# Optimization experiments

Hardware: AMD Instinct MI355X
Metric: run time of the kernel (lower is better)

Reference implementation:

```python
import jax, jax.numpy as jnp
import numpy as np

BH, S, D = 16, 2048, 128  # batch*heads, seq_len, head_dim


def setup_inputs() -> dict:
    key = jax.random.key(0)
    kq, kk, kv = jax.random.split(key, 3)
    q = jax.random.normal(kq, (BH, S, D), dtype=jnp.float32)
    k = jax.random.normal(kk, (BH, S, D), dtype=jnp.float32)
    v = jax.random.normal(kv, (BH, S, D), dtype=jnp.float32)
    # causal mask, True = masked (matches torch masked_fill_ semantics);
    # broadcast to the required [BH, S, S] shape per the module's assert.
    causal = jnp.triu(jnp.ones((S, S), dtype=jnp.bool_), k=1)
    attn_mask = jnp.broadcast_to(causal, (BH, S, S))
    return {"q": q, "k": k, "v": v, "attn_mask": attn_mask}


def reference(q, k, v, attn_mask):
    # NOTE: original module applies NO 1/sqrt(d) scaling despite its name.
    attn = jnp.einsum("bqd,bkd->bqk", q, k)              # [BH, S, S]
    attn = jnp.where(attn_mask, -jnp.inf, attn)
    attn = jax.nn.softmax(attn, axis=-1)
    # dropout is identity in eval mode
    out = jnp.einsum("bqk,bkd->bqd", attn, v)            # [BH, S, D]
    return out * q, attn                                  # faithful quirk: output * q
```

## Files before the change

### kernel.cpp

```cpp
#include <hip/hip_runtime.h>

#define BH_ 16
#define S_ 2048
#define D_ 128
#define KB_ 64
#define QB_ 64

typedef __attribute__((ext_vector_type(4))) float f32x4;
typedef __attribute__((ext_vector_type(8))) short bf16x8;
typedef unsigned short ushort_t;

__device__ __forceinline__ unsigned short f2bf(float x) {
  union { float f; unsigned int u; } v; v.f = x;
  unsigned int r = v.u + 0x7fffu + ((v.u >> 16) & 1u);
  return (unsigned short)(r >> 16);
}
__device__ __forceinline__ float bf2f(unsigned short b) {
  union { float f; unsigned int u; } v; v.u = ((unsigned int)b) << 16;
  return v.f;
}

__global__ __launch_bounds__(256) void convKfrag(const float* __restrict__ K,
                                                 ushort_t* __restrict__ KH,
                                                 ushort_t* __restrict__ KL) {
  const int tid = threadIdx.x;
  const int seg = tid >> 6;
  const int tl  = tid & 63;
  const int kt = blockIdx.x, bh = blockIdx.y;
  const float* src0 = K + ((size_t)bh * S_ + kt * 64 + (tl & 15)) * D_ +
                      seg * 32 + (tl >> 4) * 8;
  char* dh = (char*)KH + ((size_t)(bh * 32 + kt) * 16 + seg * 4) * 1024 + tl * 16;
  char* dl = (char*)KL + ((size_t)(bh * 32 + kt) * 16 + seg * 4) * 1024 + tl * 16;
#pragma unroll
  for (int t = 0; t < 4; ++t) {
    const float* src = src0 + (size_t)t * 16 * D_;
    float4 a = *(const float4*)src;
    float4 b = *(const float4*)(src + 4);
    float xs[8] = {a.x, a.y, a.z, a.w, b.x, b.y, b.z, b.w};
    union { ushort_t u[8]; uint4 v; } H, L;
#pragma unroll
    for (int j = 0; j < 8; ++j) {
      unsigned short h = f2bf(xs[j]);
      H.u[j] = h;
      L.u[j] = f2bf(xs[j] - bf2f(h));
    }
    *(uint4*)(dh + t * 1024) = H.v;
    *(uint4*)(dl + t * 1024) = L.v;
  }
}

__global__ __launch_bounds__(256) void convVfrag(const float* __restrict__ V,
                                                 ushort_t* __restrict__ VF) {
  __shared__ ushort_t tile[64][136];
  const int tid = threadIdx.x;
  const int kt = blockIdx.x, bh = blockIdx.y;
  const float* Vb = V + ((size_t)bh * S_ + kt * 64) * D_;
#pragma unroll
  for (int it = 0; it < 8; ++it) {
    int idx = it * 256 + tid;
    int fl = idx * 4;
    int s = fl >> 7, d = fl & 127;
    float4 f = *(const float4*)(Vb + (size_t)s * D_ + d);
    tile[s][d + 0] = f2bf(f.x);
    tile[s][d + 1] = f2bf(f.y);
    tile[s][d + 2] = f2bf(f.z);
    tile[s][d + 3] = f2bf(f.w);
  }
  __syncthreads();
  char* dst0 = (char*)VF + (size_t)(bh * 32 + kt) * 16384;
#pragma unroll
  for (int j = 0; j < 4; ++j) {
    int ci = j * 256 + tid;
    int l = ci & 63, fid = ci >> 6;
    int ks = fid >> 3, dt = fid & 7;
    int s0 = ks * 32 + (l >> 4) * 8;
    int d = dt * 16 + (l & 15);
    union { ushort_t u[8]; uint4 v; } T;
#pragma unroll
    for (int i = 0; i < 8; ++i) T.u[i] = tile[s0 + i][d];
    *(uint4*)(dst0 + (size_t)fid * 1024 + l * 16) = T.v;
  }
}

__global__ __launch_bounds__(256) void sdpa_fused(
    const float* __restrict__ Q, const ushort_t* __restrict__ KH,
    const ushort_t* __restrict__ KL, const ushort_t* __restrict__ VF,
    float* __restrict__ out, float* __restrict__ attn) {
  __shared__ ushort_t els[32 * 1024];
  __shared__ float rsLDS[4][16];

  const int tid = threadIdx.x, w = tid >> 6, lane = tid & 63;
  const int g = lane >> 4, c = lane & 15;

  const int bid = blockIdx.x;
  const int xcd = bid & 7, slot = bid >> 3;
  const int bh = xcd + 8 * (slot >> 7);
  const int rt = 127 - (slot & 127);
  const int q0 = rt * 16;
  const int nk = (rt >> 2) + 1;

  const float* Qb = Q + (size_t)bh * S_ * D_;
  const char* KHb = (const char*)KH + (size_t)bh * 32 * 16384;
  const char* KLb = (const char*)KL + (size_t)bh * 32 * 16384;
  const char* VFb = (const char*)VF + (size_t)bh * 32 * 16384;
  float* outb  = out  + (size_t)bh * S_ * D_;
  float* attnb = attn + (size_t)bh * S_ * S_;

  bf16x8 qhi[4], qlo[4];
  {
    const float* qrow = Qb + (size_t)(q0 + c) * D_;
#pragma unroll
    for (int ch = 0; ch < 4; ++ch) {
      const float* src = qrow + ch * 32 + g * 8;
      float4 a = *(const float4*)src;
      float4 b = *(const float4*)(src + 4);
      float xs[8] = {a.x, a.y, a.z, a.w, b.x, b.y, b.z, b.w};
#pragma unroll
      for (int i = 0; i < 8; ++i) {
        unsigned short h = f2bf(xs[i]);
        qhi[ch][i] = (short)h;
        qlo[ch][i] = (short)f2bf(xs[i] - bf2f(h));
      }
    }
  }

  const f32x4 zero4 = {0.f, 0.f, 0.f, 0.f};
  f32x4 oacc[8];
  float rs[4] = {0.f, 0.f, 0.f, 0.f};
#pragma unroll
  for (int dt = 0; dt < 8; ++dt) oacc[dt] = zero4;

  for (int kt = w; kt < nk; kt += 4) {
    const char* kth = KHb + (size_t)kt * 16384 + lane * 16;
    const char* ktl = KLb + (size_t)kt * 16384 + lane * 16;
    const char* ktv = VFb + (size_t)kt * 16384 + lane * 16;

    f32x4 acc[4];
#pragma unroll
    for (int t = 0; t < 4; ++t) acc[t] = zero4;
#pragma unroll
    for (int c2 = 0; c2 < 4; ++c2) {
      bf16x8 kh[4], kl[4];
#pragma unroll
      for (int t = 0; t < 4; ++t) {
        kh[t] = *(const bf16x8*)(kth + (c2 * 4 + t) * 1024);
        kl[t] = *(const bf16x8*)(ktl + (c2 * 4 + t) * 1024);
      }
#pragma unroll
      for (int t = 0; t < 4; ++t)
        acc[t] = __builtin_amdgcn_mfma_f32_16x16x32_bf16(qhi[c2], kh[t], acc[t], 0, 0, 0);
#pragma unroll
      for (int t = 0; t < 4; ++t)
        acc[t] = __builtin_amdgcn_mfma_f32_16x16x32_bf16(qlo[c2], kh[t], acc[t], 0, 0, 0);
#pragma unroll
      for (int t = 0; t < 4; ++t)
        acc[t] = __builtin_amdgcn_mfma_f32_16x16x32_bf16(qhi[c2], kl[t], acc[t], 0, 0, 0);
    }

#pragma unroll
    for (int r2 = 0; r2 < 4; ++r2) {
      int qrow = g * 4 + r2;
      int qg = q0 + qrow;
#pragma unroll
      for (int t = 0; t < 4; ++t) {
        int kc = t * 16 + c;
        int kg = kt * 64 + kc;
        float e = (kg <= qg) ? __expf(acc[t][r2]) : 0.f;
        rs[r2] += e;
        int off = kt * 2048 + qrow * 128 + ((kc * 2) ^ ((qrow & 7) << 4));
        *(ushort_t*)((char*)els + off) = f2bf(e);
      }
    }

    bf16x8 pa[2];
#pragma unroll
    for (int ks = 0; ks < 2; ++ks) {
      int off = kt * 2048 + c * 128 + ((ks * 64 + g * 16) ^ ((c & 7) << 4));
      pa[ks] = *(const bf16x8*)((const char*)els + off);
    }
#pragma unroll
    for (int ks = 0; ks < 2; ++ks) {
#pragma unroll
      for (int dt = 0; dt < 8; ++dt) {
        bf16x8 vf = *(const bf16x8*)(ktv + (ks * 8 + dt) * 1024);
        oacc[dt] = __builtin_amdgcn_mfma_f32_16x16x32_bf16(pa[ks], vf, oacc[dt], 0, 0, 0);
      }
    }
  }

#pragma unroll
  for (int r2 = 0; r2 < 4; ++r2) {
    float s0 = rs[r2];
#pragma unroll
    for (int m = 1; m <= 8; m <<= 1) s0 += __shfl_xor(s0, m, 64);
    if (c == 0) rsLDS[w][g * 4 + r2] = s0;
  }
  __syncthreads();

  {
    float ivr[4];
#pragma unroll
    for (int rr = 0; rr < 4; ++rr) {
      int r = w * 4 + rr;
      ivr[rr] = 1.0f / (rsLDS[0][r] + rsLDS[1][r] + rsLDS[2][r] + rsLDS[3][r]);
    }
#pragma unroll
    for (int rr = 0; rr < 4; ++rr) {
      const int r = w * 4 + rr;
      const float iv = ivr[rr];
      float* arow = attnb + (size_t)(q0 + r) * S_;
#pragma unroll
      for (int it = 0; it < 4; ++it) {
        int kb8 = it * 512 + lane * 8;
        float4 o0, o1;
        if ((kb8 >> 6) < nk) {
          const char* src = (const char*)els + (kb8 >> 6) * 2048 + r * 128 +
                            (((kb8 & 63) * 2) ^ ((r & 7) << 4));
          bf16x8 ev = *(const bf16x8*)src;
          o0.x = bf2f((ushort_t)ev[0]) * iv; o0.y = bf2f((ushort_t)ev[1]) * iv;
          o0.z = bf2f((ushort_t)ev[2]) * iv; o0.w = bf2f((ushort_t)ev[3]) * iv;
          o1.x = bf2f((ushort_t)ev[4]) * iv; o1.y = bf2f((ushort_t)ev[5]) * iv;
          o1.z = bf2f((ushort_t)ev[6]) * iv; o1.w = bf2f((ushort_t)ev[7]) * iv;
        } else {
          o0 = make_float4(0.f, 0.f, 0.f, 0.f);
          o1 = o0;
        }
        *(float4*)(arow + kb8) = o0;
        *(float4*)(arow + kb8 + 4) = o1;
      }
    }
  }
  __syncthreads();

  if (w > 0) {
    char* base = (char*)els + (size_t)(w - 1) * 8192 + lane * 128;
#pragma unroll
    for (int dt = 0; dt < 8; ++dt)
      *(f32x4*)(base + ((dt * 16) ^ ((lane & 7) << 4))) = oacc[dt];
  }
  __syncthreads();
  if (w == 0) {
    float ivr2[4];
#pragma unroll
    for (int r2 = 0; r2 < 4; ++r2) {
      int r = g * 4 + r2;
      ivr2[r2] = 1.0f / (rsLDS[0][r] + rsLDS[1][r] + rsLDS[2][r] + rsLDS[3][r]);
    }
#pragma unroll
    for (int dt = 0; dt < 8; ++dt) {
      f32x4 o = oacc[dt];
#pragma unroll
      for (int j = 0; j < 3; ++j)
        o += *(const f32x4*)((const char*)els + (size_t)j * 8192 + lane * 128 +
                             ((dt * 16) ^ ((lane & 7) << 4)));
      int d = dt * 16 + c;
#pragma unroll
      for (int r2 = 0; r2 < 4; ++r2) {
        int qg = q0 + g * 4 + r2;
        outb[(size_t)qg * D_ + d] = o[r2] * ivr2[r2] * Qb[(size_t)qg * D_ + d];
      }
    }
  }
}

__global__ __launch_bounds__(256, 2)
void sdpa_fallback(const float* __restrict__ Q, const float* __restrict__ K,
                   const float* __restrict__ V, float* __restrict__ out,
                   float* __restrict__ attn)
{
  __shared__ unsigned short khi[KB_ * D_];
  __shared__ unsigned short klo[KB_ * D_];
  __shared__ unsigned short vts[D_ * KB_];
  __shared__ unsigned short pls[4][16 * KB_];

  const int tid  = threadIdx.x;
  const int w    = tid >> 6;
  const int lane = tid & 63;
  const int g    = lane >> 4;
  const int c    = lane & 15;

  const int bh = blockIdx.y;
  const int qb = (int)gridDim.x - 1 - (int)blockIdx.x;
  const int q0 = qb * QB_;

  const float* Qb = Q + (size_t)bh * S_ * D_;
  const float* Kb = K + (size_t)bh * S_ * D_;
  const float* Vb = V + (size_t)bh * S_ * D_;
  float* outb  = out  + (size_t)bh * S_ * D_;
  float* attnb = attn + (size_t)bh * S_ * S_;

  {
    const int colstart = q0 + QB_;
    for (int r = 0; r < QB_; ++r) {
      float* rowp = attnb + (size_t)(q0 + r) * S_;
      for (int col = colstart + tid * 4; col < S_; col += 1024)
        *(float4*)(rowp + col) = make_float4(0.f, 0.f, 0.f, 0.f);
    }
  }

  bf16x8 qhi[4], qlo[4];
  {
    const float* qrow = Qb + (size_t)(q0 + w * 16 + c) * D_;
#pragma unroll
    for (int ch = 0; ch < 4; ++ch) {
      const float* src = qrow + ch * 32 + g * 8;
      float4 a = *(const float4*)src;
      float4 b = *(const float4*)(src + 4);
      float xs[8] = {a.x, a.y, a.z, a.w, b.x, b.y, b.z, b.w};
#pragma unroll
      for (int i = 0; i < 8; ++i) {
        unsigned short h = f2bf(xs[i]);
        unsigned short l = f2bf(xs[i] - bf2f(h));
        qhi[ch][i] = (short)h;
        qlo[ch][i] = (short)l;
      }
    }
  }

  auto stageK = [&](int kb) {
#pragma unroll
    for (int rr = 0; rr < 8; ++rr) {
      int flat = tid * 4 + rr * 1024;
      int kj = flat >> 7, d0 = flat & 127;
      const float* src = Kb + (size_t)(kb * KB_ + kj) * D_ + d0;
      float4 f = *(const float4*)src;
      unsigned short h0 = f2bf(f.x), h1 = f2bf(f.y), h2 = f2bf(f.z), h3 = f2bf(f.w);
      unsigned short l0 = f2bf(f.x - bf2f(h0)), l1 = f2bf(f.y - bf2f(h1));
      unsigned short l2 = f2bf(f.z - bf2f(h2)), l3 = f2bf(f.w - bf2f(h3));
      int off = kj * 256 + ((d0 * 2) ^ ((kj & 7) << 4));
      *(uint2*)((char*)khi + off) =
          make_uint2((unsigned)h0 | ((unsigned)h1 << 16), (unsigned)h2 | ((unsigned)h3 << 16));
      *(uint2*)((char*)klo + off) =
          make_uint2((unsigned)l0 | ((unsigned)l1 << 16), (unsigned)l2 | ((unsigned)l3 << 16));
    }
  };

  const f32x4 zero4 = {0.f, 0.f, 0.f, 0.f};
  auto computeS = [&](f32x4* acc) {
#pragma unroll
    for (int t = 0; t < 4; ++t) {
      acc[t] = zero4;
      int row = t * 16 + c;
      int rbase = row * 256;
      int sw = (row & 7) << 4;
#pragma unroll
      for (int c2 = 0; c2 < 4; ++c2) {
        int off = rbase + ((c2 * 64 + g * 16) ^ sw);
        bf16x8 kh_ = *(const bf16x8*)((const char*)khi + off);
        bf16x8 kl_ = *(const bf16x8*)((const char*)klo + off);
        acc[t] = __builtin_amdgcn_mfma_f32_16x16x32_bf16(qhi[c2], kh_, acc[t], 0, 0, 0);
        acc[t] = __builtin_amdgcn_mfma_f32_16x16x32_bf16(qhi[c2], kl_, acc[t], 0, 0, 0);
        acc[t] = __builtin_amdgcn_mfma_f32_16x16x32_bf16(qlo[c2], kh_, acc[t], 0, 0, 0);
      }
    }
  };

  float rsum[4] = {0.f, 0.f, 0.f, 0.f};
  for (int kb = 0; kb <= qb; ++kb) {
    __syncthreads();
    stageK(kb);
    __syncthreads();
    f32x4 acc[4];
    computeS(acc);
#pragma unroll
    for (int r2 = 0; r2 < 4; ++r2) {
      int qg = q0 + w * 16 + g * 4 + r2;
      float s0 = 0.f;
#pragma unroll
      for (int t = 0; t < 4; ++t) {
        int kg = kb * KB_ + t * 16 + c;
        float e = (kg <= qg) ? __expf(acc[t][r2]) : 0.f;
        s0 += e;
      }
#pragma unroll
      for (int m = 1; m <= 8; m <<= 1) s0 += __shfl_xor(s0, m, 64);
      rsum[r2] += s0;
    }
  }
  float invl[4];
#pragma unroll
  for (int r2 = 0; r2 < 4; ++r2) invl[r2] = 1.0f / rsum[r2];

  f32x4 oacc[8];
#pragma unroll
  for (int dt = 0; dt < 8; ++dt) oacc[dt] = zero4;

  for (int kb = 0; kb <= qb; ++kb) {
    __syncthreads();
    stageK(kb);
#pragma unroll
    for (int rr = 0; rr < 8; ++rr) {
      int d0 = 4 * (w + 4 * rr);
      const float* src = Vb + (size_t)(kb * KB_ + lane) * D_ + d0;
      float4 f = *(const float4*)src;
      float xs[4] = {f.x, f.y, f.z, f.w};
#pragma unroll
      for (int i = 0; i < 4; ++i) {
        int d = d0 + i;
        int off = d * 128 + ((lane * 2) ^ ((d & 7) << 4));
        *(unsigned short*)((char*)vts + off) = f2bf(xs[i]);
      }
    }
    __syncthreads();

    f32x4 acc[4];
    computeS(acc);

#pragma unroll
    for (int r2 = 0; r2 < 4; ++r2) {
      int qrow = g * 4 + r2;
      int qg = q0 + w * 16 + qrow;
#pragma unroll
      for (int t = 0; t < 4; ++t) {
        int kc = t * 16 + c;
        int kg = kb * KB_ + kc;
        float p = (kg <= qg) ? __expf(acc[t][r2]) * invl[r2] : 0.f;
        attnb[(size_t)qg * S_ + kg] = p;
        int off = qrow * 128 + ((kc * 2) ^ ((qrow & 7) << 4));
        *(unsigned short*)((char*)pls[w] + off) = f2bf(p);
      }
    }
    __syncthreads();

    bf16x8 pa[2];
#pragma unroll
    for (int ks = 0; ks < 2; ++ks) {
      int off = c * 128 + ((ks * 64 + g * 16) ^ ((c & 7) << 4));
      pa[ks] = *(const bf16x8*)((const char*)pls[w] + off);
    }
#pragma unroll
    for (int dt = 0; dt < 8; ++dt) {
      int d = dt * 16 + c;
      int rbase = d * 128;
      int sw = (d & 7) << 4;
#pragma unroll
      for (int ks = 0; ks < 2; ++ks) {
        int off = rbase + ((ks * 64 + g * 16) ^ sw);
        bf16x8 vf = *(const bf16x8*)((const char*)vts + off);
        oacc[dt] = __builtin_amdgcn_mfma_f32_16x16x32_bf16(pa[ks], vf, oacc[dt], 0, 0, 0);
      }
    }
  }

#pragma unroll
  for (int dt = 0; dt < 8; ++dt) {
#pragma unroll
    for (int r2 = 0; r2 < 4; ++r2) {
      int qg = q0 + w * 16 + g * 4 + r2;
      int d = dt * 16 + c;
      float qv = Qb[(size_t)qg * D_ + d];
      outb[(size_t)qg * D_ + d] = oacc[dt][r2] * qv;
    }
  }
}

extern "C" void kernel_launch(void* const* d_in, const int* in_sizes, int n_in,
                              void* d_out, int out_size, void* d_ws, size_t ws_size,
                              hipStream_t stream) {
  const float* q = (const float*)d_in[0];
  const float* k = (const float*)d_in[1];
  const float* v = (const float*)d_in[2];
  float* out  = (float*)d_out;
  float* attn = out + (size_t)BH_ * S_ * D_;

  const size_t nKV = (size_t)BH_ * S_ * D_;
  const size_t need = nKV * 2 * 3;

  if (ws_size >= need) {
    ushort_t* KH = (ushort_t*)d_ws;
    ushort_t* KL = KH + nKV;
    ushort_t* VF = KL + nKV;

    convKfrag<<<dim3(S_ / 64, BH_), dim3(256), 0, stream>>>(k, KH, KL);
    convVfrag<<<dim3(S_ / 64, BH_), dim3(256), 0, stream>>>(v, VF);
    sdpa_fused<<<dim3(BH_ * 128), dim3(256), 0, stream>>>(q, KH, KL, VF, out, attn);
  } else {
    sdpa_fallback<<<dim3(S_ / QB_, BH_), dim3(256), 0, stream>>>(q, k, v, out, attn);
  }
}
```

Before: 133.4 us.

## Use 32-row query tiles with paired causal rows in 512-thread blocks

Replaces the 16-row, 4-wave fused attention kernel with a 32-row, 8-wave kernel. Each block processes two query tiles, p and 63-p, so causal work is balanced across a fixed grid of 512 blocks. Each K fragment loaded from global memory now feeds two 16-row MFMA groups, which halves K traffic per query row. The output reduction across waves is moved to an LDS park-and-sum with vectorised float4 stores. In exchange, the kernel uses 128KB of LDS, which probably limits it to one block per CU despite the launch bound, and it adds extra barriers per tile.

```diff
diff --git a/kernel.cpp b/kernel.cpp
--- a/kernel.cpp
+++ b/kernel.cpp
@@ -82,22 +82,19 @@
   }
 }
 
-__global__ __launch_bounds__(256) void sdpa_fused(
+__global__ __launch_bounds__(512, 2) void sdpa_fused32(
     const float* __restrict__ Q, const ushort_t* __restrict__ KH,
     const ushort_t* __restrict__ KL, const ushort_t* __restrict__ VF,
     float* __restrict__ out, float* __restrict__ attn) {
-  __shared__ ushort_t els[32 * 1024];
-  __shared__ float rsLDS[4][16];
+  __shared__ ushort_t els[65536];
+  __shared__ float rsLDS[8][32];
 
   const int tid = threadIdx.x, w = tid >> 6, lane = tid & 63;
   const int g = lane >> 4, c = lane & 15;
 
   const int bid = blockIdx.x;
-  const int xcd = bid & 7, slot = bid >> 3;
-  const int bh = xcd + 8 * (slot >> 7);
-  const int rt = 127 - (slot & 127);
-  const int q0 = rt * 16;
-  const int nk = (rt >> 2) + 1;
+  const int bh = (bid & 7) + 8 * ((bid >> 3) & 1);
+  const int p = bid >> 4;
 
   const float* Qb = Q + (size_t)bh * S_ * D_;
   const char* KHb = (const char*)KH + (size_t)bh * 32 * 16384;
@@ -106,115 +103,140 @@
   float* outb  = out  + (size_t)bh * S_ * D_;
   float* attnb = attn + (size_t)bh * S_ * S_;
 
-  bf16x8 qhi[4], qlo[4];
-  {
-    const float* qrow = Qb + (size_t)(q0 + c) * D_;
-#pragma unroll
-    for (int ch = 0; ch < 4; ++ch) {
-      const float* src = qrow + ch * 32 + g * 8;
-      float4 a = *(const float4*)src;
-      float4 b = *(const float4*)(src + 4);
-      float xs[8] = {a.x, a.y, a.z, a.w, b.x, b.y, b.z, b.w};
-#pragma unroll
-      for (int i = 0; i < 8; ++i) {
-        unsigned short h = f2bf(xs[i]);
-        qhi[ch][i] = (short)h;
-        qlo[ch][i] = (short)f2bf(xs[i] - bf2f(h));
-      }
-    }
-  }
-
   const f32x4 zero4 = {0.f, 0.f, 0.f, 0.f};
-  f32x4 oacc[8];
-  float rs[4] = {0.f, 0.f, 0.f, 0.f};
-#pragma unroll
-  for (int dt = 0; dt < 8; ++dt) oacc[dt] = zero4;
-
-  for (int kt = w; kt < nk; kt += 4) {
-    const char* kth = KHb + (size_t)kt * 16384 + lane * 16;
-    const char* ktl = KLb + (size_t)kt * 16384 + lane * 16;
-    const char* ktv = VFb + (size_t)kt * 16384 + lane * 16;
-
-    f32x4 acc[4];
-#pragma unroll
-    for (int t = 0; t < 4; ++t) acc[t] = zero4;
-#pragma unroll
-    for (int c2 = 0; c2 < 4; ++c2) {
-      bf16x8 kh[4], kl[4];
-#pragma unroll
-      for (int t = 0; t < 4; ++t) {
-        kh[t] = *(const bf16x8*)(kth + (c2 * 4 + t) * 1024);
-        kl[t] = *(const bf16x8*)(ktl + (c2 * 4 + t) * 1024);
-      }
-#pragma unroll
-      for (int t = 0; t < 4; ++t)
-        acc[t] = __builtin_amdgcn_mfma_f32_16x16x32_bf16(qhi[c2], kh[t], acc[t], 0, 0, 0);
-#pragma unroll
-      for (int t = 0; t < 4; ++t)
-        acc[t] = __builtin_amdgcn_mfma_f32_16x16x32_bf16(qlo[c2], kh[t], acc[t], 0, 0, 0);
-#pragma unroll
-      for (int t = 0; t < 4; ++t)
-        acc[t] = __builtin_amdgcn_mfma_f32_16x16x32_bf16(qhi[c2], kl[t], acc[t], 0, 0, 0);
-    }
-
-#pragma unroll
-    for (int r2 = 0; r2 < 4; ++r2) {
-      int qrow = g * 4 + r2;
-      int qg = q0 + qrow;
-#pragma unroll
-      for (int t = 0; t < 4; ++t) {
-        int kc = t * 16 + c;
-        int kg = kt * 64 + kc;
-        float e = (kg <= qg) ? __expf(acc[t][r2]) : 0.f;
-        rs[r2] += e;
-        int off = kt * 2048 + qrow * 128 + ((kc * 2) ^ ((qrow & 7) << 4));
-        *(ushort_t*)((char*)els + off) = f2bf(e);
-      }
-    }
-
-    bf16x8 pa[2];
-#pragma unroll
-    for (int ks = 0; ks < 2; ++ks) {
-      int off = kt * 2048 + c * 128 + ((ks * 64 + g * 16) ^ ((c & 7) << 4));
-      pa[ks] = *(const bf16x8*)((const char*)els + off);
-    }
-#pragma unroll
-    for (int ks = 0; ks < 2; ++ks) {
-#pragma unroll
-      for (int dt = 0; dt < 8; ++dt) {
-        bf16x8 vf = *(const bf16x8*)(ktv + (ks * 8 + dt) * 1024);
-        oacc[dt] = __builtin_amdgcn_mfma_f32_16x16x32_bf16(pa[ks], vf, oacc[dt], 0, 0, 0);
-      }
-    }
-  }
-
-#pragma unroll
-  for (int r2 = 0; r2 < 4; ++r2) {
-    float s0 = rs[r2];
-#pragma unroll
-    for (int m = 1; m <= 8; m <<= 1) s0 += __shfl_xor(s0, m, 64);
-    if (c == 0) rsLDS[w][g * 4 + r2] = s0;
-  }
-  __syncthreads();
-
-  {
-    float ivr[4];
-#pragma unroll
-    for (int rr = 0; rr < 4; ++rr) {
-      int r = w * 4 + rr;
-      ivr[rr] = 1.0f / (rsLDS[0][r] + rsLDS[1][r] + rsLDS[2][r] + rsLDS[3][r]);
-    }
+
+#pragma unroll 1
+  for (int which = 0; which < 2; ++which) {
+    const int rt = which ? p : 63 - p;
+    const int q0 = rt * 32;
+    const int nk = ((rt * 32 + 31) >> 6) + 1;
+
+    bf16x8 qhi[2][4], qlo[2][4];
+#pragma unroll
+    for (int h = 0; h < 2; ++h) {
+      const float* qrow = Qb + (size_t)(q0 + h * 16 + c) * D_;
+#pragma unroll
+      for (int ch = 0; ch < 4; ++ch) {
+        const float* src = qrow + ch * 32 + g * 8;
+        float4 a = *(const float4*)src;
+        float4 b = *(const float4*)(src + 4);
+        float xs[8] = {a.x, a.y, a.z, a.w, b.x, b.y, b.z, b.w};
+#pragma unroll
+        for (int i = 0; i < 8; ++i) {
+          unsigned short hh = f2bf(xs[i]);
+          qhi[h][ch][i] = (short)hh;
+          qlo[h][ch][i] = (short)f2bf(xs[i] - bf2f(hh));
+        }
+      }
+    }
+
+    f32x4 oacc[2][8];
+    float rs[2][4];
+#pragma unroll
+    for (int h = 0; h < 2; ++h) {
+#pragma unroll
+      for (int dt = 0; dt < 8; ++dt) oacc[h][dt] = zero4;
+#pragma unroll
+      for (int r2 = 0; r2 < 4; ++r2) rs[h][r2] = 0.f;
+    }
+
+    for (int kt = w; kt < nk; kt += 8) {
+      const char* kth = KHb + (size_t)kt * 16384 + lane * 16;
+      const char* ktl = KLb + (size_t)kt * 16384 + lane * 16;
+      const char* ktv = VFb + (size_t)kt * 16384 + lane * 16;
+
+      f32x4 acc[2][4];
+#pragma unroll
+      for (int h = 0; h < 2; ++h)
+#pragma unroll
+        for (int t = 0; t < 4; ++t) acc[h][t] = zero4;
+
+#pragma unroll
+      for (int c2 = 0; c2 < 4; ++c2) {
+        bf16x8 kh[4], kl[4];
+#pragma unroll
+        for (int t = 0; t < 4; ++t) {
+          kh[t] = *(const bf16x8*)(kth + (c2 * 4 + t) * 1024);
+          kl[t] = *(const bf16x8*)(ktl + (c2 * 4 + t) * 1024);
+        }
+#pragma unroll
+        for (int h = 0; h < 2; ++h)
+#pragma unroll
+          for (int t = 0; t < 4; ++t)
+            acc[h][t] = __builtin_amdgcn_mfma_f32_16x16x32_bf16(qhi[h][c2], kh[t], acc[h][t], 0, 0, 0);
+#pragma unroll
+        for (int h = 0; h < 2; ++h)
+#pragma unroll
+          for (int t = 0; t < 4; ++t)
+            acc[h][t] = __builtin_amdgcn_mfma_f32_16x16x32_bf16(qlo[h][c2], kh[t], acc[h][t], 0, 0, 0);
+#pragma unroll
+        for (int h = 0; h < 2; ++h)
+#pragma unroll
+          for (int t = 0; t < 4; ++t)
+            acc[h][t] = __builtin_amdgcn_mfma_f32_16x16x32_bf16(qhi[h][c2], kl[t], acc[h][t], 0, 0, 0);
+      }
+
+#pragma unroll
+      for (int h = 0; h < 2; ++h) {
+#pragma unroll
+        for (int r2 = 0; r2 < 4; ++r2) {
+          int qrow = g * 4 + r2;
+          int qg = q0 + h * 16 + qrow;
+#pragma unroll
+          for (int t = 0; t < 4; ++t) {
+            int kc = t * 16 + c;
+            int kg = kt * 64 + kc;
+            float e = (kg <= qg) ? __expf(acc[h][t][r2]) : 0.f;
+            rs[h][r2] += e;
+            int off = kt * 4096 + (h * 16 + qrow) * 128 +
+                      ((kc * 2) ^ ((qrow & 7) << 4));
+            *(ushort_t*)((char*)els + off) = f2bf(e);
+          }
+        }
+      }
+
+#pragma unroll
+      for (int ks = 0; ks < 2; ++ks) {
+        int sw = (c & 7) << 4;
+        bf16x8 pa0 = *(const bf16x8*)((const char*)els + kt * 4096 +
+                                      c * 128 + ((ks * 64 + g * 16) ^ sw));
+        bf16x8 pa1 = *(const bf16x8*)((const char*)els + kt * 4096 +
+                                      (16 + c) * 128 + ((ks * 64 + g * 16) ^ sw));
+#pragma unroll
+        for (int dt = 0; dt < 8; ++dt) {
+          bf16x8 vf = *(const bf16x8*)(ktv + (ks * 8 + dt) * 1024);
+          oacc[0][dt] = __builtin_amdgcn_mfma_f32_16x16x32_bf16(pa0, vf, oacc[0][dt], 0, 0, 0);
+          oacc[1][dt] = __builtin_amdgcn_mfma_f32_16x16x32_bf16(pa1, vf, oacc[1][dt], 0, 0, 0);
+        }
+      }
+    }
+
+#pragma unroll
+    for (int h = 0; h < 2; ++h) {
+#pragma unroll
+      for (int r2 = 0; r2 < 4; ++r2) {
+        float s0 = rs[h][r2];
+#pragma unroll
+        for (int m = 1; m <= 8; m <<= 1) s0 += __shfl_xor(s0, m, 64);
+        if (c == 0) rsLDS[w][h * 16 + g * 4 + r2] = s0;
+      }
+    }
+    __syncthreads();
+
 #pragma unroll
     for (int rr = 0; rr < 4; ++rr) {
       const int r = w * 4 + rr;
-      const float iv = ivr[rr];
+      float l = 0.f;
+#pragma unroll
+      for (int j = 0; j < 8; ++j) l += rsLDS[j][r];
+      const float iv = 1.0f / l;
       float* arow = attnb + (size_t)(q0 + r) * S_;
 #pragma unroll
       for (int it = 0; it < 4; ++it) {
         int kb8 = it * 512 + lane * 8;
         float4 o0, o1;
         if ((kb8 >> 6) < nk) {
-          const char* src = (const char*)els + (kb8 >> 6) * 2048 + r * 128 +
+          const char* src = (const char*)els + (kb8 >> 6) * 4096 + r * 128 +
                             (((kb8 & 63) * 2) ^ ((r & 7) << 4));
           bf16x8 ev = *(const bf16x8*)src;
           o0.x = bf2f((ushort_t)ev[0]) * iv; o0.y = bf2f((ushort_t)ev[1]) * iv;
@@ -229,37 +251,47 @@
         *(float4*)(arow + kb8 + 4) = o1;
       }
     }
-  }
-  __syncthreads();
-
-  if (w > 0) {
-    char* base = (char*)els + (size_t)(w - 1) * 8192 + lane * 128;
-#pragma unroll
-    for (int dt = 0; dt < 8; ++dt)
-      *(f32x4*)(base + ((dt * 16) ^ ((lane & 7) << 4))) = oacc[dt];
-  }
-  __syncthreads();
-  if (w == 0) {
-    float ivr2[4];
-#pragma unroll
-    for (int r2 = 0; r2 < 4; ++r2) {
-      int r = g * 4 + r2;
-      ivr2[r2] = 1.0f / (rsLDS[0][r] + rsLDS[1][r] + rsLDS[2][r] + rsLDS[3][r]);
-    }
-#pragma unroll
-    for (int dt = 0; dt < 8; ++dt) {
-      f32x4 o = oacc[dt];
-#pragma unroll
-      for (int j = 0; j < 3; ++j)
-        o += *(const f32x4*)((const char*)els + (size_t)j * 8192 + lane * 128 +
-                             ((dt * 16) ^ ((lane & 7) << 4)));
-      int d = dt * 16 + c;
-#pragma unroll
-      for (int r2 = 0; r2 < 4; ++r2) {
-        int qg = q0 + g * 4 + r2;
-        outb[(size_t)qg * D_ + d] = o[r2] * ivr2[r2] * Qb[(size_t)qg * D_ + d];
-      }
-    }
+    __syncthreads();
+
+    {
+      char* park = (char*)els + (size_t)w * 16384;
+#pragma unroll
+      for (int h = 0; h < 2; ++h) {
+#pragma unroll
+        for (int dt = 0; dt < 8; ++dt) {
+#pragma unroll
+          for (int r2 = 0; r2 < 4; ++r2) {
+            int row = h * 16 + g * 4 + r2;
+            int d = dt * 16 + c;
+            *(float*)(park + row * 512 + ((d * 4) ^ ((row & 7) << 4))) =
+                oacc[h][dt][r2];
+          }
+        }
+      }
+    }
+    __syncthreads();
+
+#pragma unroll
+    for (int rr = 0; rr < 2; ++rr) {
+      int row = w * 4 + rr * 2 + (lane >> 5);
+      int d0 = (lane & 31) * 4;
+      int boff = row * 512 + ((d0 * 4) ^ ((row & 7) << 4));
+      f32x4 o = zero4;
+#pragma unroll
+      for (int j = 0; j < 8; ++j)
+        o += *(const f32x4*)((const char*)els + (size_t)j * 16384 + boff);
+      float l = 0.f;
+#pragma unroll
+      for (int j = 0; j < 8; ++j) l += rsLDS[j][row];
+      const float iv = 1.0f / l;
+      int qg = q0 + row;
+      float4 qv = *(const float4*)(Qb + (size_t)qg * D_ + d0);
+      float4 res;
+      res.x = o[0] * iv * qv.x; res.y = o[1] * iv * qv.y;
+      res.z = o[2] * iv * qv.z; res.w = o[3] * iv * qv.w;
+      *(float4*)(outb + (size_t)qg * D_ + d0) = res;
+    }
+    __syncthreads();
   }
 }
 
@@ -473,7 +505,7 @@
 
     convKfrag<<<dim3(S_ / 64, BH_), dim3(256), 0, stream>>>(k, KH, KL);
     convVfrag<<<dim3(S_ / 64, BH_), dim3(256), 0, stream>>>(v, VF);
-    sdpa_fused<<<dim3(BH_ * 128), dim3(256), 0, stream>>>(q, KH, KL, VF, out, attn);
+    sdpa_fused32<<<dim3(512), dim3(512), 0, stream>>>(q, KH, KL, VF, out, attn);
   } else {
     sdpa_fallback<<<dim3(S_ / QB_, BH_), dim3(256), 0, stream>>>(q, k, v, out, attn);
   }
```

Measured after the change: 201.4 us. +50.9%, slower.
